# Kernel tuning notes

Measured on AMD Instinct MI355X. Metric: run time of the kernel, lower is better.

## Reference

```python
import jax, jax.numpy as jnp
import numpy as np

H = 50  # hidden size
I = 1   # input size


def setup_inputs() -> dict:
    key = jax.random.key(0)
    ks = jax.random.split(key, 7)
    B, T = 4096, 512
    s = 1.0 / np.sqrt(H)  # PyTorch default init scale
    x = jax.random.normal(ks[0], (B, T, I), dtype=jnp.float32)
    W_ih = jax.random.uniform(ks[1], (4 * H, I), jnp.float32, -s, s)
    W_hh = jax.random.uniform(ks[2], (4 * H, H), jnp.float32, -s, s)
    b_ih = jax.random.uniform(ks[3], (4 * H,), jnp.float32, -s, s)
    b_hh = jax.random.uniform(ks[4], (4 * H,), jnp.float32, -s, s)
    W_out = jax.random.uniform(ks[5], (1, H), jnp.float32, -s, s)
    b_out = jax.random.uniform(ks[6], (1,), jnp.float32, -s, s)
    return {"x": x, "W_ih": W_ih, "W_hh": W_hh, "b_ih": b_ih,
            "b_hh": b_hh, "W_out": W_out, "b_out": b_out}


def _lstm(x, W_ih, W_hh, b_ih, b_hh):
    # x: [B, T, I]; gate order in PyTorch: i, f, g, o
    B = x.shape[0]
    b = b_ih + b_hh
    # precompute input projection for all timesteps: [T, B, 4H]
    xg = jnp.einsum('bti,gi->tbg', x, W_ih) + b

    def step(carry, xg_t):
        h, c = carry
        gates = xg_t + h @ W_hh.T  # [B, 4H]
        i, f, g, o = jnp.split(gates, 4, axis=-1)
        c = jax.nn.sigmoid(f) * c + jax.nn.sigmoid(i) * jnp.tanh(g)
        h = jax.nn.sigmoid(o) * jnp.tanh(c)
        return (h, c), h

    h0 = jnp.zeros((B, H), x.dtype)
    c0 = jnp.zeros((B, H), x.dtype)
    _, hs = jax.lax.scan(step, (h0, c0), xg)  # hs: [T, B, H]
    return hs.transpose(1, 0, 2)  # [B, T, H]


def reference(x, W_ih, W_hh, b_ih, b_hh, W_out, b_out):
    h = _lstm(x, W_ih, W_hh, b_ih, b_hh)          # [B, T, H]
    return h @ W_out.T + b_out                     # [B, T, 1]
```

## Files before the change

kernel.cpp:

```cpp
#include <hip/hip_runtime.h>
#include <math.h>

#define HID 50
#define TT  512
#define BT  16
#define NCW 7
#define NTH 512
#define HS  72
#define L2E 1.44269504088896f
#define K2C 2.88539008177793f

typedef __attribute__((ext_vector_type(8))) short bf16x8;
typedef __attribute__((ext_vector_type(4))) float f32x4;

__device__ __forceinline__ unsigned short bf16_rtne(float f) {
    unsigned u = __float_as_uint(f);
    u = (u + 0x7FFFu + ((u >> 16) & 1u)) >> 16;
    return (unsigned short)u;
}
__device__ __forceinline__ float bf16_f32(unsigned short s) {
    return __uint_as_float(((unsigned)s) << 16);
}

__global__ __launch_bounds__(NTH, 1) void lstm_mfma17_kernel(
    const float* __restrict__ x,
    const float* __restrict__ W_ih,
    const float* __restrict__ W_hh,
    const float* __restrict__ b_ih,
    const float* __restrict__ b_hh,
    const float* __restrict__ W_out,
    const float* __restrict__ b_out,
    float* __restrict__ out)
{
    const int tid  = threadIdx.x;
    const int lane = tid & 63;
    const int wv   = tid >> 6;
    const int col  = lane & 15;
    const int quad = lane >> 4;

    __shared__ __align__(16) unsigned short Hh[2][BT][HS];

    for (int i = tid; i < 2 * BT * HS; i += NTH)
        (&Hh[0][0][0])[i] = 0;

    bf16x8 Ah[2][2];
    float cs0 = 0.f, cs1 = 0.f;
    const int uoa = (wv * 2) * 4 + quad;
    const int uob = (wv * 2 + 1) * 4 + quad;
    const int uo2a = (uoa < HID) ? uoa : uoa + 5;
    const int uo2b = (uob < HID) ? uob : uob + 5;

    if (wv < NCW) {
        #pragma unroll
        for (int i = 0; i < 2; ++i) {
            const int gh  = (wv * 2 + i) * 16 + col;
            const int u   = gh >> 2;
            const int ty  = gh & 3;
            const bool vl = (u < HID);
            const int og  = ty * HID + u;
            const float sc = (ty == 2) ? K2C : L2E;
            #pragma unroll
            for (int kk = 0; kk < 2; ++kk) {
                #pragma unroll
                for (int j = 0; j < 8; ++j) {
                    const int k = kk * 32 + quad * 8 + j;
                    float v = 0.f;
                    if (vl) {
                        if (k < HID)      v = sc * W_hh[og * HID + k];
                        else if (k == 50) v = sc * W_ih[og];
                        else if (k == 51) v = sc * (b_ih[og] + b_hh[og]);
                        else if (k == 52) v = sc * W_ih[og];
                        else if (k == 53) {
                            const float sb = sc * (b_ih[og] + b_hh[og]);
                            v = sb - bf16_f32(bf16_rtne(sb));
                        } else if (k == 54) {
                            const float sw = sc * W_ih[og];
                            v = sw - bf16_f32(bf16_rtne(sw));
                        }
                    }
                    Ah[i][kk][j] = (short)bf16_rtne(v);
                }
            }
        }
    } else {
        #pragma unroll
        for (int kk = 0; kk < 2; ++kk) {
            #pragma unroll
            for (int j = 0; j < 8; ++j) {
                const int k = kk * 32 + quad * 8 + j;
                const float v = (k < HID) ? W_out[k] : 0.f;
                const unsigned short hi = bf16_rtne(v);
                short val = 0;
                if (col == 0)      val = (short)hi;
                else if (col == 1) val = (short)bf16_rtne(v - bf16_f32(hi));
                Ah[0][kk][j] = val;
                Ah[1][kk][j] = 0;
            }
        }
    }
    const float bo = b_out[0];
    float* yout = out + (size_t)blockIdx.x * BT * TT + (size_t)(lane & 15) * TT;

    const int xb = (lane >= 16) ? (lane - 16) : 0;
    const float* xrow = x + (size_t)(blockIdx.x * BT + xb) * TT;
    float xa = 0.f;
    if (wv == NCW && lane >= 16 && lane < 32)
        xa = xrow[1];

    __syncthreads();

    if (tid < BT) {
        const float x0 = x[(size_t)(blockIdx.x * BT + tid) * TT];
        const unsigned short hx = bf16_rtne(x0);
        const unsigned short lx = bf16_rtne(x0 - bf16_f32(hx));
        unsigned* row32 = (unsigned*)&Hh[0][tid][0];
        row32[25] = (unsigned)hx | (0x3F80u << 16);
        row32[26] = (unsigned)lx | (0x3F80u << 16);
        Hh[0][tid][54] = hx;
    }
    __syncthreads();

    const unsigned short* rdA = &Hh[0][col][quad * 8];
    const unsigned short* rdB = &Hh[1][col][quad * 8];
    unsigned short* wrA0 = &Hh[1][col][uo2a];
    unsigned short* wrA1 = &Hh[1][col][uo2b];
    unsigned short* wrB0 = &Hh[0][col][uo2a];
    unsigned short* wrB1 = &Hh[0][col][uo2b];
    unsigned* xwA = (unsigned*)&Hh[1][xb][0];
    unsigned* xwB = (unsigned*)&Hh[0][xb][0];
    const f32x4 z = {0.f, 0.f, 0.f, 0.f};

#define GATES(ACC, CS, HOUT)                                                  \
    do {                                                                      \
        const float Ei = __builtin_amdgcn_exp2f(-(ACC).x);                    \
        const float Ef = __builtin_amdgcn_exp2f(-(ACC).y);                    \
        const float Eg = __builtin_amdgcn_exp2f((ACC).z);                     \
        const float Eo = __builtin_amdgcn_exp2f(-(ACC).w);                    \
        const float DIG = (1.f + Ei) * (1.f + Eg);                            \
        const float DF  = 1.f + Ef;                                           \
        const float t1  = fmaf(K2C, Eg, -K2C);                                \
        const float num = fmaf((CS), DIG, t1 * DF);                           \
        (CS) = num * __builtin_amdgcn_rcpf(DF * DIG);                         \
        const float Ec = __builtin_amdgcn_exp2f(CS);                          \
        (HOUT) = (Ec - 1.f) *                                                 \
                 __builtin_amdgcn_rcpf((1.f + Eo) * (1.f + Ec));              \
    } while (0)

#define LSTM_STEP(RD, WR0, WR1, XW, TI)                                       \
    do {                                                                      \
        if (wv < NCW) {                                                       \
            const bf16x8 B0 = *(const bf16x8*)(RD);                           \
            const bf16x8 B1 = *(const bf16x8*)((RD) + 32);                    \
            f32x4 a0 = __builtin_amdgcn_mfma_f32_16x16x32_bf16(Ah[0][0], B0, z, 0, 0, 0); \
            f32x4 a1 = __builtin_amdgcn_mfma_f32_16x16x32_bf16(Ah[1][0], B0, z, 0, 0, 0); \
            a0 = __builtin_amdgcn_mfma_f32_16x16x32_bf16(Ah[0][1], B1, a0, 0, 0, 0); \
            a1 = __builtin_amdgcn_mfma_f32_16x16x32_bf16(Ah[1][1], B1, a1, 0, 0, 0); \
            float h0, h1;                                                     \
            GATES(a0, cs0, h0);                                               \
            GATES(a1, cs1, h1);                                               \
            unsigned hpk;                                                     \
            asm("v_cvt_pk_bf16_f32 %0, %1, %2" : "=v"(hpk) : "v"(h0), "v"(h1)); \
            *(WR0) = (unsigned short)(hpk & 0xFFFFu);                         \
            *(WR1) = (unsigned short)(hpk >> 16);                             \
        } else {                                                              \
            const bf16x8 B0 = *(const bf16x8*)(RD);                           \
            const bf16x8 B1 = *(const bf16x8*)((RD) + 32);                    \
            if (lane >= 16 && lane < 32) {                                    \
                const unsigned short hx = bf16_rtne(xa);                      \
                const unsigned short lx = bf16_rtne(xa - bf16_f32(hx));       \
                (XW)[25] = (unsigned)hx | (0x3F80u << 16);                    \
                (XW)[26] = (unsigned)lx | (0x3F80u << 16);                    \
                ((unsigned short*)(XW))[54] = hx;                             \
                xa = xrow[((TI) + 2 < TT) ? (TI) + 2 : TT - 1];               \
            }                                                                 \
            f32x4 a0 = __builtin_amdgcn_mfma_f32_16x16x32_bf16(Ah[0][0], B0, z, 0, 0, 0); \
            a0 = __builtin_amdgcn_mfma_f32_16x16x32_bf16(Ah[0][1], B1, a0, 0, 0, 0); \
            if (lane < 16 && (TI) > 0)                                        \
                yout[(TI) - 1] = a0.x + a0.y + bo;                            \
        }                                                                     \
    } while (0)

    for (int t = 0; t < TT; t += 2) {
        LSTM_STEP(rdA, wrA0, wrA1, xwA, t);
        asm volatile("s_waitcnt lgkmcnt(0)\n\ts_barrier" ::: "memory");
        LSTM_STEP(rdB, wrB0, wrB1, xwB, t + 1);
        asm volatile("s_waitcnt lgkmcnt(0)\n\ts_barrier" ::: "memory");
    }
#undef LSTM_STEP
#undef GATES

    if (wv == NCW) {
        const bf16x8 B0 = *(const bf16x8*)rdA;
        const bf16x8 B1 = *(const bf16x8*)(rdA + 32);
        f32x4 a0 = __builtin_amdgcn_mfma_f32_16x16x32_bf16(Ah[0][0], B0, z, 0, 0, 0);
        a0 = __builtin_amdgcn_mfma_f32_16x16x32_bf16(Ah[0][1], B1, a0, 0, 0, 0);
        if (lane < 16)
            yout[TT - 1] = a0.x + a0.y + bo;
    }
}

extern "C" void kernel_launch(void* const* d_in, const int* in_sizes, int n_in,
                              void* d_out, int out_size, void* d_ws, size_t ws_size,
                              hipStream_t stream) {
    const float* x     = (const float*)d_in[0];
    const float* W_ih  = (const float*)d_in[1];
    const float* W_hh  = (const float*)d_in[2];
    const float* b_ih  = (const float*)d_in[3];
    const float* b_hh  = (const float*)d_in[4];
    const float* W_out = (const float*)d_in[5];
    const float* b_out = (const float*)d_in[6];
    float* out = (float*)d_out;

    const int B = in_sizes[0] / TT;
    lstm_mfma17_kernel<<<B / BT, NTH, 0, stream>>>(x, W_ih, W_hh, b_ih, b_hh,
                                                   W_out, b_out, out);
}
```

Baseline: 232.0 us.

## Fold output projection and x staging into the last gate wave, dropping the eighth wave

The dedicated eighth wave, which computed the output projection and staged the next x values into shared memory, is removed. Wave 6's second gate tile was unused padding (units 56+ beyond the hidden size), so it now holds the W_out hi/lo weights, and wave 6 also writes the x values and the output. The block drops from 8 to 7 waves, which means fewer participants in the per-step barrier. In exchange, wave 6 carries extra x-staging and output-store work on its critical path every step.

```diff
diff --git a/kernel.cpp b/kernel.cpp
--- a/kernel.cpp
+++ b/kernel.cpp
@@ -5,7 +5,7 @@
 #define TT  512
 #define BT  16
 #define NCW 7
-#define NTH 512
+#define NTH 448
 #define HS  72
 #define L2E 1.44269504088896f
 #define K2C 2.88539008177793f
@@ -22,7 +22,7 @@
     return __uint_as_float(((unsigned)s) << 16);
 }
 
-__global__ __launch_bounds__(NTH, 1) void lstm_mfma17_kernel(
+__global__ __launch_bounds__(NTH, 1) void lstm_mfma18_kernel(
     const float* __restrict__ x,
     const float* __restrict__ W_ih,
     const float* __restrict__ W_hh,
@@ -50,9 +50,24 @@
     const int uo2a = (uoa < HID) ? uoa : uoa + 5;
     const int uo2b = (uob < HID) ? uob : uob + 5;
 
-    if (wv < NCW) {
-        #pragma unroll
-        for (int i = 0; i < 2; ++i) {
+    #pragma unroll
+    for (int i = 0; i < 2; ++i) {
+        if (wv == 6 && i == 1) {
+            #pragma unroll
+            for (int kk = 0; kk < 2; ++kk) {
+                #pragma unroll
+                for (int j = 0; j < 8; ++j) {
+                    const int k = kk * 32 + quad * 8 + j;
+                    float v = 0.f;
+                    if (k < HID) {
+                        const float w = W_out[k];
+                        if (col == 0)      v = w;
+                        else if (col == 1) v = w - bf16_f32(bf16_rtne(w));
+                    }
+                    Ah[1][kk][j] = (short)bf16_rtne(v);
+                }
+            }
+        } else {
             const int gh  = (wv * 2 + i) * 16 + col;
             const int u   = gh >> 2;
             const int ty  = gh & 3;
@@ -82,29 +97,13 @@
                 }
             }
         }
-    } else {
-        #pragma unroll
-        for (int kk = 0; kk < 2; ++kk) {
-            #pragma unroll
-            for (int j = 0; j < 8; ++j) {
-                const int k = kk * 32 + quad * 8 + j;
-                const float v = (k < HID) ? W_out[k] : 0.f;
-                const unsigned short hi = bf16_rtne(v);
-                short val = 0;
-                if (col == 0)      val = (short)hi;
-                else if (col == 1) val = (short)bf16_rtne(v - bf16_f32(hi));
-                Ah[0][kk][j] = val;
-                Ah[1][kk][j] = 0;
-            }
-        }
     }
     const float bo = b_out[0];
-    float* yout = out + (size_t)blockIdx.x * BT * TT + (size_t)(lane & 15) * TT;
-
-    const int xb = (lane >= 16) ? (lane - 16) : 0;
-    const float* xrow = x + (size_t)(blockIdx.x * BT + xb) * TT;
+    float* yout = out + (size_t)blockIdx.x * BT * TT + (size_t)col * TT;
+
+    const float* xrow = x + (size_t)(blockIdx.x * BT + col) * TT;
     float xa = 0.f;
-    if (wv == NCW && lane >= 16 && lane < 32)
+    if (wv == 6 && lane >= 48)
         xa = xrow[1];
 
     __syncthreads();
@@ -126,8 +125,8 @@
     unsigned short* wrA1 = &Hh[1][col][uo2b];
     unsigned short* wrB0 = &Hh[0][col][uo2a];
     unsigned short* wrB1 = &Hh[0][col][uo2b];
-    unsigned* xwA = (unsigned*)&Hh[1][xb][0];
-    unsigned* xwB = (unsigned*)&Hh[0][xb][0];
+    unsigned* xwA = (unsigned*)&Hh[1][col][0];
+    unsigned* xwB = (unsigned*)&Hh[0][col][0];
     const f32x4 z = {0.f, 0.f, 0.f, 0.f};
 
 #define GATES(ACC, CS, HOUT)                                                  \
@@ -148,36 +147,29 @@
 
 #define LSTM_STEP(RD, WR0, WR1, XW, TI)                                       \
     do {                                                                      \
-        if (wv < NCW) {                                                       \
-            const bf16x8 B0 = *(const bf16x8*)(RD);                           \
-            const bf16x8 B1 = *(const bf16x8*)((RD) + 32);                    \
-            f32x4 a0 = __builtin_amdgcn_mfma_f32_16x16x32_bf16(Ah[0][0], B0, z, 0, 0, 0); \
-            f32x4 a1 = __builtin_amdgcn_mfma_f32_16x16x32_bf16(Ah[1][0], B0, z, 0, 0, 0); \
-            a0 = __builtin_amdgcn_mfma_f32_16x16x32_bf16(Ah[0][1], B1, a0, 0, 0, 0); \
-            a1 = __builtin_amdgcn_mfma_f32_16x16x32_bf16(Ah[1][1], B1, a1, 0, 0, 0); \
-            float h0, h1;                                                     \
-            GATES(a0, cs0, h0);                                               \
-            GATES(a1, cs1, h1);                                               \
-            unsigned hpk;                                                     \
-            asm("v_cvt_pk_bf16_f32 %0, %1, %2" : "=v"(hpk) : "v"(h0), "v"(h1)); \
-            *(WR0) = (unsigned short)(hpk & 0xFFFFu);                         \
-            *(WR1) = (unsigned short)(hpk >> 16);                             \
-        } else {                                                              \
-            const bf16x8 B0 = *(const bf16x8*)(RD);                           \
-            const bf16x8 B1 = *(const bf16x8*)((RD) + 32);                    \
-            if (lane >= 16 && lane < 32) {                                    \
-                const unsigned short hx = bf16_rtne(xa);                      \
-                const unsigned short lx = bf16_rtne(xa - bf16_f32(hx));       \
-                (XW)[25] = (unsigned)hx | (0x3F80u << 16);                    \
-                (XW)[26] = (unsigned)lx | (0x3F80u << 16);                    \
-                ((unsigned short*)(XW))[54] = hx;                             \
-                xa = xrow[((TI) + 2 < TT) ? (TI) + 2 : TT - 1];               \
-            }                                                                 \
-            f32x4 a0 = __builtin_amdgcn_mfma_f32_16x16x32_bf16(Ah[0][0], B0, z, 0, 0, 0); \
-            a0 = __builtin_amdgcn_mfma_f32_16x16x32_bf16(Ah[0][1], B1, a0, 0, 0, 0); \
-            if (lane < 16 && (TI) > 0)                                        \
-                yout[(TI) - 1] = a0.x + a0.y + bo;                            \
+        const bf16x8 B0 = *(const bf16x8*)(RD);                               \
+        const bf16x8 B1 = *(const bf16x8*)((RD) + 32);                        \
+        if (wv == 6 && lane >= 48) {                                          \
+            const unsigned short hx = bf16_rtne(xa);                          \
+            const unsigned short lx = bf16_rtne(xa - bf16_f32(hx));           \
+            (XW)[25] = (unsigned)hx | (0x3F80u << 16);                        \
+            (XW)[26] = (unsigned)lx | (0x3F80u << 16);                        \
+            ((unsigned short*)(XW))[54] = hx;                                 \
+            xa = xrow[((TI) + 2 < TT) ? (TI) + 2 : TT - 1];                   \
         }                                                                     \
+        f32x4 a0 = __builtin_amdgcn_mfma_f32_16x16x32_bf16(Ah[0][0], B0, z, 0, 0, 0); \
+        f32x4 a1 = __builtin_amdgcn_mfma_f32_16x16x32_bf16(Ah[1][0], B0, z, 0, 0, 0); \
+        a0 = __builtin_amdgcn_mfma_f32_16x16x32_bf16(Ah[0][1], B1, a0, 0, 0, 0); \
+        a1 = __builtin_amdgcn_mfma_f32_16x16x32_bf16(Ah[1][1], B1, a1, 0, 0, 0); \
+        float h0, h1;                                                         \
+        GATES(a0, cs0, h0);                                                   \
+        GATES(a1, cs1, h1);                                                   \
+        unsigned hpk;                                                         \
+        asm("v_cvt_pk_bf16_f32 %0, %1, %2" : "=v"(hpk) : "v"(h0), "v"(h1));   \
+        *(WR0) = (unsigned short)(hpk & 0xFFFFu);                             \
+        *(WR1) = (unsigned short)(hpk >> 16);                                 \
+        if (wv == 6 && lane < 16 && (TI) > 0)                                 \
+            yout[(TI) - 1] = a1.x + a1.y + bo;                                \
     } while (0)
 
     for (int t = 0; t < TT; t += 2) {
@@ -189,13 +181,13 @@
 #undef LSTM_STEP
 #undef GATES
 
-    if (wv == NCW) {
+    if (wv == 6) {
         const bf16x8 B0 = *(const bf16x8*)rdA;
         const bf16x8 B1 = *(const bf16x8*)(rdA + 32);
-        f32x4 a0 = __builtin_amdgcn_mfma_f32_16x16x32_bf16(Ah[0][0], B0, z, 0, 0, 0);
-        a0 = __builtin_amdgcn_mfma_f32_16x16x32_bf16(Ah[0][1], B1, a0, 0, 0, 0);
+        f32x4 a1 = __builtin_amdgcn_mfma_f32_16x16x32_bf16(Ah[1][0], B0, z, 0, 0, 0);
+        a1 = __builtin_amdgcn_mfma_f32_16x16x32_bf16(Ah[1][1], B1, a1, 0, 0, 0);
         if (lane < 16)
-            yout[TT - 1] = a0.x + a0.y + bo;
+            yout[TT - 1] = a1.x + a1.y + bo;
     }
 }
 
@@ -212,6 +204,6 @@
     float* out = (float*)d_out;
 
     const int B = in_sizes[0] / TT;
-    lstm_mfma17_kernel<<<B / BT, NTH, 0, stream>>>(x, W_ih, W_hh, b_ih, b_hh,
+    lstm_mfma18_kernel<<<B / BT, NTH, 0, stream>>>(x, W_ih, W_hh, b_ih, b_hh,
                                                    W_out, b_out, out);
 }
```

Result: slower. 255.0 us (+9.9%).

## Fold last two hidden units into output wave, drop to seven waves

Applied to the files above, without the earlier changes.

Before, seven compute waves covered 56 unit slots, six of them padding, and an eighth wave handled the output projection and the x staging. Now six compute waves cover units 0-47. The output wave packs W_out rows plus the gate rows for units 48 and 49 into one MFMA A operand, so its single matmul also computes their gates. This cuts the block from 512 to 448 threads, so each per-step barrier has fewer waves to wait for. In exchange the output wave does more serial work every step (gates plus the output sum and the x staging), which may lengthen the critical path.

```diff
diff --git a/kernel.cpp b/kernel.cpp
--- a/kernel.cpp
+++ b/kernel.cpp
@@ -4,8 +4,7 @@
 #define HID 50
 #define TT  512
 #define BT  16
-#define NCW 7
-#define NTH 512
+#define NTH 448
 #define HS  72
 #define L2E 1.44269504088896f
 #define K2C 2.88539008177793f
@@ -22,7 +21,7 @@
     return __uint_as_float(((unsigned)s) << 16);
 }
 
-__global__ __launch_bounds__(NTH, 1) void lstm_mfma17_kernel(
+__global__ __launch_bounds__(NTH, 1) void lstm_mfma19_kernel(
     const float* __restrict__ x,
     const float* __restrict__ W_ih,
     const float* __restrict__ W_hh,
@@ -45,18 +44,18 @@
 
     bf16x8 Ah[2][2];
     float cs0 = 0.f, cs1 = 0.f;
-    const int uoa = (wv * 2) * 4 + quad;
-    const int uob = (wv * 2 + 1) * 4 + quad;
-    const int uo2a = (uoa < HID) ? uoa : uoa + 5;
-    const int uo2b = (uob < HID) ? uob : uob + 5;
-
-    if (wv < NCW) {
+    const int uoa = wv * 8 + quad;
+    const int uob = wv * 8 + 4 + quad;
+    const int uom = (quad == 1) ? 48 : (quad == 2) ? 49 : (quad == 0) ? 55 : 56;
+    const int s0 = (wv < 6) ? uoa : uom;
+    const int s1 = (wv < 6) ? uob : 57;
+
+    if (wv < 6) {
         #pragma unroll
         for (int i = 0; i < 2; ++i) {
             const int gh  = (wv * 2 + i) * 16 + col;
             const int u   = gh >> 2;
             const int ty  = gh & 3;
-            const bool vl = (u < HID);
             const int og  = ty * HID + u;
             const float sc = (ty == 2) ? K2C : L2E;
             #pragma unroll
@@ -65,18 +64,16 @@
                 for (int j = 0; j < 8; ++j) {
                     const int k = kk * 32 + quad * 8 + j;
                     float v = 0.f;
-                    if (vl) {
-                        if (k < HID)      v = sc * W_hh[og * HID + k];
-                        else if (k == 50) v = sc * W_ih[og];
-                        else if (k == 51) v = sc * (b_ih[og] + b_hh[og]);
-                        else if (k == 52) v = sc * W_ih[og];
-                        else if (k == 53) {
-                            const float sb = sc * (b_ih[og] + b_hh[og]);
-                            v = sb - bf16_f32(bf16_rtne(sb));
-                        } else if (k == 54) {
-                            const float sw = sc * W_ih[og];
-                            v = sw - bf16_f32(bf16_rtne(sw));
-                        }
+                    if (k < HID)      v = sc * W_hh[og * HID + k];
+                    else if (k == 50) v = sc * W_ih[og];
+                    else if (k == 51) v = sc * (b_ih[og] + b_hh[og]);
+                    else if (k == 52) v = sc * W_ih[og];
+                    else if (k == 53) {
+                        const float sb = sc * (b_ih[og] + b_hh[og]);
+                        v = sb - bf16_f32(bf16_rtne(sb));
+                    } else if (k == 54) {
+                        const float sw = sc * W_ih[og];
+                        v = sw - bf16_f32(bf16_rtne(sw));
                     }
                     Ah[i][kk][j] = (short)bf16_rtne(v);
                 }
@@ -88,23 +85,40 @@
             #pragma unroll
             for (int j = 0; j < 8; ++j) {
                 const int k = kk * 32 + quad * 8 + j;
-                const float v = (k < HID) ? W_out[k] : 0.f;
-                const unsigned short hi = bf16_rtne(v);
-                short val = 0;
-                if (col == 0)      val = (short)hi;
-                else if (col == 1) val = (short)bf16_rtne(v - bf16_f32(hi));
-                Ah[0][kk][j] = val;
+                float v = 0.f;
+                if (col < 2) {
+                    if (k < HID) {
+                        const float w = W_out[k];
+                        v = (col == 0) ? w : w - bf16_f32(bf16_rtne(w));
+                    }
+                } else if (col >= 4 && col < 12) {
+                    const int u  = (col < 8) ? 48 : 49;
+                    const int ty = col & 3;
+                    const int og = ty * HID + u;
+                    const float sc = (ty == 2) ? K2C : L2E;
+                    if (k < HID)      v = sc * W_hh[og * HID + k];
+                    else if (k == 50) v = sc * W_ih[og];
+                    else if (k == 51) v = sc * (b_ih[og] + b_hh[og]);
+                    else if (k == 52) v = sc * W_ih[og];
+                    else if (k == 53) {
+                        const float sb = sc * (b_ih[og] + b_hh[og]);
+                        v = sb - bf16_f32(bf16_rtne(sb));
+                    } else if (k == 54) {
+                        const float sw = sc * W_ih[og];
+                        v = sw - bf16_f32(bf16_rtne(sw));
+                    }
+                }
+                Ah[0][kk][j] = (short)bf16_rtne(v);
                 Ah[1][kk][j] = 0;
             }
         }
     }
     const float bo = b_out[0];
-    float* yout = out + (size_t)blockIdx.x * BT * TT + (size_t)(lane & 15) * TT;
-
-    const int xb = (lane >= 16) ? (lane - 16) : 0;
-    const float* xrow = x + (size_t)(blockIdx.x * BT + xb) * TT;
+    float* yout = out + (size_t)blockIdx.x * BT * TT + (size_t)col * TT;
+
+    const float* xrow = x + (size_t)(blockIdx.x * BT + col) * TT;
     float xa = 0.f;
-    if (wv == NCW && lane >= 16 && lane < 32)
+    if (wv == 6 && lane >= 48)
         xa = xrow[1];
 
     __syncthreads();
@@ -122,12 +136,12 @@
 
     const unsigned short* rdA = &Hh[0][col][quad * 8];
     const unsigned short* rdB = &Hh[1][col][quad * 8];
-    unsigned short* wrA0 = &Hh[1][col][uo2a];
-    unsigned short* wrA1 = &Hh[1][col][uo2b];
-    unsigned short* wrB0 = &Hh[0][col][uo2a];
-    unsigned short* wrB1 = &Hh[0][col][uo2b];
-    unsigned* xwA = (unsigned*)&Hh[1][xb][0];
-    unsigned* xwB = (unsigned*)&Hh[0][xb][0];
+    unsigned short* wrA0 = &Hh[1][col][s0];
+    unsigned short* wrA1 = &Hh[1][col][s1];
+    unsigned short* wrB0 = &Hh[0][col][s0];
+    unsigned short* wrB1 = &Hh[0][col][s1];
+    unsigned* xwA = (unsigned*)&Hh[1][col][0];
+    unsigned* xwB = (unsigned*)&Hh[0][col][0];
     const f32x4 z = {0.f, 0.f, 0.f, 0.f};
 
 #define GATES(ACC, CS, HOUT)                                                  \
@@ -148,9 +162,9 @@
 
 #define LSTM_STEP(RD, WR0, WR1, XW, TI)                                       \
     do {                                                                      \
-        if (wv < NCW) {                                                       \
-            const bf16x8 B0 = *(const bf16x8*)(RD);                           \
-            const bf16x8 B1 = *(const bf16x8*)((RD) + 32);                    \
+        const bf16x8 B0 = *(const bf16x8*)(RD);                               \
+        const bf16x8 B1 = *(const bf16x8*)((RD) + 32);                        \
+        if (wv < 6) {                                                         \
             f32x4 a0 = __builtin_amdgcn_mfma_f32_16x16x32_bf16(Ah[0][0], B0, z, 0, 0, 0); \
             f32x4 a1 = __builtin_amdgcn_mfma_f32_16x16x32_bf16(Ah[1][0], B0, z, 0, 0, 0); \
             a0 = __builtin_amdgcn_mfma_f32_16x16x32_bf16(Ah[0][1], B1, a0, 0, 0, 0); \
@@ -163,9 +177,7 @@
             *(WR0) = (unsigned short)(hpk & 0xFFFFu);                         \
             *(WR1) = (unsigned short)(hpk >> 16);                             \
         } else {                                                              \
-            const bf16x8 B0 = *(const bf16x8*)(RD);                           \
-            const bf16x8 B1 = *(const bf16x8*)((RD) + 32);                    \
-            if (lane >= 16 && lane < 32) {                                    \
+            if (lane >= 48) {                                                 \
                 const unsigned short hx = bf16_rtne(xa);                      \
                 const unsigned short lx = bf16_rtne(xa - bf16_f32(hx));       \
                 (XW)[25] = (unsigned)hx | (0x3F80u << 16);                    \
@@ -175,6 +187,11 @@
             }                                                                 \
             f32x4 a0 = __builtin_amdgcn_mfma_f32_16x16x32_bf16(Ah[0][0], B0, z, 0, 0, 0); \
             a0 = __builtin_amdgcn_mfma_f32_16x16x32_bf16(Ah[0][1], B1, a0, 0, 0, 0); \
+            float h0;                                                         \
+            GATES(a0, cs0, h0);                                               \
+            unsigned hpk;                                                     \
+            asm("v_cvt_pk_bf16_f32 %0, %1, %2" : "=v"(hpk) : "v"(h0), "v"(h0)); \
+            *(WR0) = (unsigned short)(hpk & 0xFFFFu);                         \
             if (lane < 16 && (TI) > 0)                                        \
                 yout[(TI) - 1] = a0.x + a0.y + bo;                            \
         }                                                                     \
@@ -189,7 +206,7 @@
 #undef LSTM_STEP
 #undef GATES
 
-    if (wv == NCW) {
+    if (wv == 6) {
         const bf16x8 B0 = *(const bf16x8*)rdA;
         const bf16x8 B1 = *(const bf16x8*)(rdA + 32);
         f32x4 a0 = __builtin_amdgcn_mfma_f32_16x16x32_bf16(Ah[0][0], B0, z, 0, 0, 0);
@@ -212,6 +229,6 @@
     float* out = (float*)d_out;
 
     const int B = in_sizes[0] / TT;
-    lstm_mfma17_kernel<<<B / BT, NTH, 0, stream>>>(x, W_ih, W_hh, b_ih, b_hh,
+    lstm_mfma19_kernel<<<B / BT, NTH, 0, stream>>>(x, W_ih, W_hh, b_ih, b_hh,
                                                    W_out, b_out, out);
 }
```

New measurement: 245.6 us. 1.06x slower.
